# Performance work log

Measured on AMD Instinct MI355X. Metric: run time of the kernel, lower is better.

Reference implementation:

```python
import jax, jax.numpy as jnp
import numpy as np

BN_EPS = 1e-5

def setup_inputs() -> dict:
    key = jax.random.key(0)
    k1, k2 = jax.random.split(key)
    B, C, H, W, K = 256, 2048, 7, 7, 16
    featmap = jax.random.normal(k1, (B, C, H, W), dtype=jnp.float32)
    w16 = jax.random.normal(k2, (K, C), dtype=jnp.float32) * 0.02  # 1x1 conv weight
    bn_gamma = jnp.ones((K,), jnp.float32)
    bn_beta = jnp.zeros((K,), jnp.float32)
    bn_mean = jnp.zeros((K,), jnp.float32)
    bn_var = jnp.ones((K,), jnp.float32)
    return {"featmap": featmap, "w16": w16, "bn_gamma": bn_gamma,
            "bn_beta": bn_beta, "bn_mean": bn_mean, "bn_var": bn_var}

def reference(featmap, w16, bn_gamma, bn_beta, bn_mean, bn_var):
    # featmap: [B, 2048, 7, 7]; 1x1 conv -> featcov16: [B, 16, 7, 7]
    featcov16 = jnp.einsum('bchw,kc->bkhw', featmap, w16)
    # BatchNorm2d(16), inference-style with running stats
    inv = bn_gamma / jnp.sqrt(bn_var + BN_EPS)
    featcov16 = featcov16 * inv[None, :, None, None] + (bn_beta - bn_mean * inv)[None, :, None, None]
    # Loop-free bilinear pooling: original repeats featcov16[:,i] to 2048 ch,
    # multiplies with featmap, and AvgPool2d(7) -> mean over HxW.
    HW = featmap.shape[2] * featmap.shape[3]
    feat_matrix = jnp.einsum('bkhw,bchw->bkc', featcov16, featmap) / HW  # [B,16,2048]
    bp_out_feat = feat_matrix.reshape(feat_matrix.shape[0], -1)  # [B, 32768]
    return bp_out_feat
```

## Files before the change

kernel.cpp:

```cpp
#include <hip/hip_runtime.h>

#define BATCH 256
#define CDIM  2048
#define HW    49
#define KDIM  16


__global__ __launch_bounds__(256) void prep_kernel(
    const float* __restrict__ w16,
    const float* __restrict__ gamma, const float* __restrict__ beta,
    const float* __restrict__ mean,  const float* __restrict__ var,
    float* __restrict__ wT, float* __restrict__ pscr)
{
    const int idx = blockIdx.x * 256 + threadIdx.x;
    if (idx < CDIM * KDIM) {
        const int c = idx >> 4, k = idx & 15;
        const float inv = gamma[k] * rsqrtf(var[k] + 1e-5f) * (1.0f / 49.0f);
        wT[idx] = w16[k * CDIM + c] * inv;
    }
    for (int i = idx; i < BATCH * (HW * KDIM); i += 256 * 256) {
        const int k = i & 15;
        const float inv   = gamma[k] * rsqrtf(var[k] + 1e-5f);
        const float shift = (beta[k] - mean[k] * inv) * (1.0f / 49.0f);
        pscr[i] = shift;
    }
}

__global__ __launch_bounds__(512) void conv_kernel(
    const float* __restrict__ fm, const float* __restrict__ wT,
    float* __restrict__ pscr)
{
    __shared__ float red[8 * KDIM * 52];

    const int tid  = threadIdx.x;
    const int b    = blockIdx.x >> 2;
    const int q    = blockIdx.x & 3;
    const int wav  = __builtin_amdgcn_readfirstlane(tid >> 6);
    const int lane = tid & 63;
    const int hwi  = lane < HW ? lane : HW - 1;
    const int cbase = q * 512 + wav * 64;

    const float*  __restrict__ fmb = fm + (size_t)b * CDIM * HW;
    const float4* __restrict__ wt4 = (const float4*)wT;

    float acc[KDIM];
    #pragma unroll
    for (int k = 0; k < KDIM; ++k) acc[k] = 0.f;

    #pragma unroll 2
    for (int g = 0; g < 64; g += 8) {
        float f[8];
        #pragma unroll
        for (int u = 0; u < 8; ++u)
            f[u] = fmb[(size_t)(cbase + g + u) * HW + hwi];
        #pragma unroll
        for (int u = 0; u < 8; ++u) {
            const int c4 = (cbase + g + u) * 4;
            const float4 w0 = wt4[c4 + 0];
            const float4 w1 = wt4[c4 + 1];
            const float4 w2 = wt4[c4 + 2];
            const float4 w3 = wt4[c4 + 3];
            const float fv = f[u];
            acc[0]  += w0.x * fv; acc[1]  += w0.y * fv; acc[2]  += w0.z * fv; acc[3]  += w0.w * fv;
            acc[4]  += w1.x * fv; acc[5]  += w1.y * fv; acc[6]  += w1.z * fv; acc[7]  += w1.w * fv;
            acc[8]  += w2.x * fv; acc[9]  += w2.y * fv; acc[10] += w2.z * fv; acc[11] += w2.w * fv;
            acc[12] += w3.x * fv; acc[13] += w3.y * fv; acc[14] += w3.z * fv; acc[15] += w3.w * fv;
        }
    }

    if (lane < HW) {
        #pragma unroll
        for (int k = 0; k < KDIM; ++k)
            red[wav * (KDIM * 52) + k * 52 + lane] = acc[k];
    }
    __syncthreads();
    for (int j = tid; j < HW * KDIM; j += 512) {
        const int k = j / HW, hw = j - k * HW;
        float s = 0.f;
        #pragma unroll
        for (int w = 0; w < 8; ++w) s += red[w * (KDIM * 52) + k * 52 + hw];
        atomicAdd(&pscr[(size_t)b * (HW * KDIM) + hw * KDIM + k], s);
    }
}

__global__ __launch_bounds__(256) void bp_kernel(
    const float* __restrict__ fm, const float* __restrict__ pscr,
    float* __restrict__ out)
{
    __shared__ __align__(16) float fs[256 * HW];

    const int tid  = threadIdx.x;
    const int b    = blockIdx.x >> 1;
    const int half = blockIdx.x & 1;

    const float*  __restrict__ fmb = fm + (size_t)b * CDIM * HW;
    const float4* __restrict__ P4  = (const float4*)(pscr + (size_t)b * (HW * KDIM));

    for (int ch = 0; ch < 4; ++ch) {
        const int cb = half * 1024 + ch * 256;
        __syncthreads();
        {
            const float4* src = (const float4*)(fmb + (size_t)cb * HW);
            float4* dst = (float4*)fs;
            for (int i = tid; i < (256 * HW) / 4; i += 256) dst[i] = src[i];
        }
        __syncthreads();

        float acc[KDIM];
        #pragma unroll
        for (int k = 0; k < KDIM; ++k) acc[k] = 0.f;

        const float* row = fs + tid * HW;
        #pragma unroll 7
        for (int hw = 0; hw < HW; ++hw) {
            const float fv = row[hw];
            const float4 p0 = P4[hw * 4 + 0];
            const float4 p1 = P4[hw * 4 + 1];
            const float4 p2 = P4[hw * 4 + 2];
            const float4 p3 = P4[hw * 4 + 3];
            acc[0]  += p0.x * fv; acc[1]  += p0.y * fv; acc[2]  += p0.z * fv; acc[3]  += p0.w * fv;
            acc[4]  += p1.x * fv; acc[5]  += p1.y * fv; acc[6]  += p1.z * fv; acc[7]  += p1.w * fv;
            acc[8]  += p2.x * fv; acc[9]  += p2.y * fv; acc[10] += p2.z * fv; acc[11] += p2.w * fv;
            acc[12] += p3.x * fv; acc[13] += p3.y * fv; acc[14] += p3.z * fv; acc[15] += p3.w * fv;
        }

        float* ob = out + (size_t)b * (KDIM * CDIM) + cb + tid;
        #pragma unroll
        for (int k = 0; k < KDIM; ++k) ob[k * CDIM] = acc[k];
    }
}

extern "C" void kernel_launch(void* const* d_in, const int* in_sizes, int n_in,
                              void* d_out, int out_size, void* d_ws, size_t ws_size,
                              hipStream_t stream) {
    const float* fm    = (const float*)d_in[0];
    const float* w16   = (const float*)d_in[1];
    const float* gamma = (const float*)d_in[2];
    const float* beta  = (const float*)d_in[3];
    const float* mean  = (const float*)d_in[4];
    const float* var   = (const float*)d_in[5];
    float* out  = (float*)d_out;
    float* wT   = (float*)d_ws;
    float* pscr = (float*)d_ws + CDIM * KDIM;

    prep_kernel<<<256, 256, 0, stream>>>(w16, gamma, beta, mean, var, wT, pscr);
    conv_kernel<<<BATCH * 4, 512, 0, stream>>>(fm, wT, pscr);
    bp_kernel<<<BATCH * 2, 256, 0, stream>>>(fm, pscr, out);
}
```

Measured before the change: 224.5 us.

## Replace conv atomics with per-strip partials, LDS direct loads, and finer bp grid

The conv kernel now splits each batch into 8 channel strips and loads each strip straight into LDS with global_load_lds. Each block writes a non-atomic partial result, and a new mid kernel sums the partials and adds the BN shift. This removes the atomicAdd contention and the pscr initialisation in the prep kernel. The bp kernel now uses 8 blocks per batch with one chunk each, which raises parallelism, at the cost of an extra kernel launch and a pass over the partial buffer.

```diff
diff --git a/kernel.cpp b/kernel.cpp
--- a/kernel.cpp
+++ b/kernel.cpp
@@ -5,82 +5,111 @@
 #define HW    49
 #define KDIM  16
 
+#define OSTRIP 8
+#define SC     256
+#define STRIP_B (SC * HW * 4)
+#define NLOAD  (STRIP_B / 1024)
+
+#define GLDS(g, l) __builtin_amdgcn_global_load_lds(                        \
+        (const __attribute__((address_space(1))) unsigned int*)(g),          \
+        (__attribute__((address_space(3))) unsigned int*)(l), 16, 0, 0)
+
 
 __global__ __launch_bounds__(256) void prep_kernel(
     const float* __restrict__ w16,
-    const float* __restrict__ gamma, const float* __restrict__ beta,
-    const float* __restrict__ mean,  const float* __restrict__ var,
-    float* __restrict__ wT, float* __restrict__ pscr)
+    const float* __restrict__ gamma, const float* __restrict__ var,
+    float* __restrict__ wT)
 {
     const int idx = blockIdx.x * 256 + threadIdx.x;
-    if (idx < CDIM * KDIM) {
-        const int c = idx >> 4, k = idx & 15;
-        const float inv = gamma[k] * rsqrtf(var[k] + 1e-5f) * (1.0f / 49.0f);
-        wT[idx] = w16[k * CDIM + c] * inv;
-    }
-    for (int i = idx; i < BATCH * (HW * KDIM); i += 256 * 256) {
-        const int k = i & 15;
-        const float inv   = gamma[k] * rsqrtf(var[k] + 1e-5f);
-        const float shift = (beta[k] - mean[k] * inv) * (1.0f / 49.0f);
-        pscr[i] = shift;
-    }
+    const int c = idx >> 4, k = idx & 15;
+    const float inv = gamma[k] * rsqrtf(var[k] + 1e-5f) * (1.0f / 49.0f);
+    wT[idx] = w16[k * CDIM + c] * inv;
 }
 
-__global__ __launch_bounds__(512) void conv_kernel(
+__global__ __launch_bounds__(256) void conv_kernel(
     const float* __restrict__ fm, const float* __restrict__ wT,
     float* __restrict__ pscr)
 {
-    __shared__ float red[8 * KDIM * 52];
+    __shared__ __align__(16) float fbuf[SC * HW + 4];
+    __shared__ __align__(16) float red[4 * KDIM * 52];
 
     const int tid  = threadIdx.x;
-    const int b    = blockIdx.x >> 2;
-    const int q    = blockIdx.x & 3;
-    const int wav  = __builtin_amdgcn_readfirstlane(tid >> 6);
+    const int b    = blockIdx.x >> 3;
+    const int o    = blockIdx.x & 7;
+    const int wavu = __builtin_amdgcn_readfirstlane(tid >> 6);
     const int lane = tid & 63;
     const int hwi  = lane < HW ? lane : HW - 1;
-    const int cbase = q * 512 + wav * 64;
 
-    const float*  __restrict__ fmb = fm + (size_t)b * CDIM * HW;
-    const float4* __restrict__ wt4 = (const float4*)wT;
+    {
+        const char* gbase = (const char*)fm
+            + (size_t)b * (CDIM * HW * 4) + (size_t)o * STRIP_B;
+        char* lbase = (char*)fbuf;
+        const int nld = (wavu == 0) ? 13 : 12;
+        for (int i = 0; i < nld; ++i) {
+            const int j = wavu + 4 * i;
+            GLDS(gbase + j * 1024 + lane * 16, lbase + j * 1024);
+        }
+    }
+    __syncthreads();
 
     float acc[KDIM];
     #pragma unroll
     for (int k = 0; k < KDIM; ++k) acc[k] = 0.f;
 
-    #pragma unroll 2
-    for (int g = 0; g < 64; g += 8) {
-        float f[8];
-        #pragma unroll
-        for (int u = 0; u < 8; ++u)
-            f[u] = fmb[(size_t)(cbase + g + u) * HW + hwi];
-        #pragma unroll
-        for (int u = 0; u < 8; ++u) {
-            const int c4 = (cbase + g + u) * 4;
-            const float4 w0 = wt4[c4 + 0];
-            const float4 w1 = wt4[c4 + 1];
-            const float4 w2 = wt4[c4 + 2];
-            const float4 w3 = wt4[c4 + 3];
-            const float fv = f[u];
-            acc[0]  += w0.x * fv; acc[1]  += w0.y * fv; acc[2]  += w0.z * fv; acc[3]  += w0.w * fv;
-            acc[4]  += w1.x * fv; acc[5]  += w1.y * fv; acc[6]  += w1.z * fv; acc[7]  += w1.w * fv;
-            acc[8]  += w2.x * fv; acc[9]  += w2.y * fv; acc[10] += w2.z * fv; acc[11] += w2.w * fv;
-            acc[12] += w3.x * fv; acc[13] += w3.y * fv; acc[14] += w3.z * fv; acc[15] += w3.w * fv;
-        }
+    const int cl0 = wavu * 64;
+    const float4* __restrict__ wq = (const float4*)(wT + (size_t)((o * SC + cl0) << 4));
+
+    #pragma unroll 8
+    for (int cc = 0; cc < 64; ++cc) {
+        const float fv = fbuf[(cl0 + cc) * HW + hwi];
+        const float4 w0 = wq[cc * 4 + 0];
+        const float4 w1 = wq[cc * 4 + 1];
+        const float4 w2 = wq[cc * 4 + 2];
+        const float4 w3 = wq[cc * 4 + 3];
+        acc[0]  += w0.x * fv; acc[1]  += w0.y * fv; acc[2]  += w0.z * fv; acc[3]  += w0.w * fv;
+        acc[4]  += w1.x * fv; acc[5]  += w1.y * fv; acc[6]  += w1.z * fv; acc[7]  += w1.w * fv;
+        acc[8]  += w2.x * fv; acc[9]  += w2.y * fv; acc[10] += w2.z * fv; acc[11] += w2.w * fv;
+        acc[12] += w3.x * fv; acc[13] += w3.y * fv; acc[14] += w3.z * fv; acc[15] += w3.w * fv;
     }
 
     if (lane < HW) {
         #pragma unroll
         for (int k = 0; k < KDIM; ++k)
-            red[wav * (KDIM * 52) + k * 52 + lane] = acc[k];
+            red[wavu * (KDIM * 52) + k * 52 + lane] = acc[k];
     }
     __syncthreads();
-    for (int j = tid; j < HW * KDIM; j += 512) {
-        const int k = j / HW, hw = j - k * HW;
-        float s = 0.f;
-        #pragma unroll
-        for (int w = 0; w < 8; ++w) s += red[w * (KDIM * 52) + k * 52 + hw];
-        atomicAdd(&pscr[(size_t)b * (HW * KDIM) + hw * KDIM + k], s);
+    for (int p = tid; p < HW * KDIM; p += 256) {
+        const int k = p / HW, hw = p - k * HW;
+        const int a = k * 52 + hw;
+        const float s = red[a] + red[a + 832] + red[a + 1664] + red[a + 2496];
+        pscr[(size_t)blockIdx.x * 784 + p] = s;
     }
+}
+
+__global__ __launch_bounds__(256) void mid_kernel(
+    float* __restrict__ pscr,
+    const float* __restrict__ gamma, const float* __restrict__ beta,
+    const float* __restrict__ mean,  const float* __restrict__ var)
+{
+    const int tid  = threadIdx.x;
+    const size_t base = (size_t)blockIdx.x * (OSTRIP * 784);
+    float s0 = 0.f, s1 = 0.f, s2 = 0.f, s3 = 0.f;
+
+#define MIDR(SV, R) { const int j = tid + 256 * (R); if (j < 784) {            \
+        const int k = j & 15, hw = j >> 4;                                     \
+        const size_t src = base + k * HW + hw;                                 \
+        float t = 0.f;                                                         \
+        _Pragma("unroll")                                                      \
+        for (int oo = 0; oo < OSTRIP; ++oo) t += pscr[src + oo * 784];         \
+        const float inv = gamma[k] * rsqrtf(var[k] + 1e-5f);                   \
+        SV = t + (beta[k] - mean[k] * inv) * (1.0f / 49.0f); } }
+    MIDR(s0, 0) MIDR(s1, 1) MIDR(s2, 2) MIDR(s3, 3)
+#undef MIDR
+    __syncthreads();
+    if (tid < 784)        pscr[base + tid]       = s0;
+    if (tid + 256 < 784)  pscr[base + tid + 256] = s1;
+    if (tid + 512 < 784)  pscr[base + tid + 512] = s2;
+    if (tid + 768 < 784)  pscr[base + tid + 768] = s3;
 }
 
 __global__ __launch_bounds__(256) void bp_kernel(
@@ -89,45 +118,40 @@
 {
     __shared__ __align__(16) float fs[256 * HW];
 
-    const int tid  = threadIdx.x;
-    const int b    = blockIdx.x >> 1;
-    const int half = blockIdx.x & 1;
+    const int tid = threadIdx.x;
+    const int b   = blockIdx.x >> 3;
+    const int oc  = (blockIdx.x & 7) * 256;
 
-    const float*  __restrict__ fmb = fm + (size_t)b * CDIM * HW;
-    const float4* __restrict__ P4  = (const float4*)(pscr + (size_t)b * (HW * KDIM));
+    {
+        const float4* src = (const float4*)(fm + ((size_t)b * CDIM + oc) * HW);
+        float4* dst = (float4*)fs;
+        for (int i = tid; i < (256 * HW) / 4; i += 256) dst[i] = src[i];
+    }
+    __syncthreads();
 
-    for (int ch = 0; ch < 4; ++ch) {
-        const int cb = half * 1024 + ch * 256;
-        __syncthreads();
-        {
-            const float4* src = (const float4*)(fmb + (size_t)cb * HW);
-            float4* dst = (float4*)fs;
-            for (int i = tid; i < (256 * HW) / 4; i += 256) dst[i] = src[i];
-        }
-        __syncthreads();
+    const float4* __restrict__ P4 = (const float4*)(pscr + (size_t)b * (OSTRIP * 784));
 
-        float acc[KDIM];
-        #pragma unroll
-        for (int k = 0; k < KDIM; ++k) acc[k] = 0.f;
+    float acc[KDIM];
+    #pragma unroll
+    for (int k = 0; k < KDIM; ++k) acc[k] = 0.f;
 
-        const float* row = fs + tid * HW;
-        #pragma unroll 7
-        for (int hw = 0; hw < HW; ++hw) {
-            const float fv = row[hw];
-            const float4 p0 = P4[hw * 4 + 0];
-            const float4 p1 = P4[hw * 4 + 1];
-            const float4 p2 = P4[hw * 4 + 2];
-            const float4 p3 = P4[hw * 4 + 3];
-            acc[0]  += p0.x * fv; acc[1]  += p0.y * fv; acc[2]  += p0.z * fv; acc[3]  += p0.w * fv;
-            acc[4]  += p1.x * fv; acc[5]  += p1.y * fv; acc[6]  += p1.z * fv; acc[7]  += p1.w * fv;
-            acc[8]  += p2.x * fv; acc[9]  += p2.y * fv; acc[10] += p2.z * fv; acc[11] += p2.w * fv;
-            acc[12] += p3.x * fv; acc[13] += p3.y * fv; acc[14] += p3.z * fv; acc[15] += p3.w * fv;
-        }
+    const float* row = fs + tid * HW;
+    #pragma unroll
+    for (int hw = 0; hw < HW; ++hw) {
+        const float fv = row[hw];
+        const float4 p0 = P4[hw * 4 + 0];
+        const float4 p1 = P4[hw * 4 + 1];
+        const float4 p2 = P4[hw * 4 + 2];
+        const float4 p3 = P4[hw * 4 + 3];
+        acc[0]  += p0.x * fv; acc[1]  += p0.y * fv; acc[2]  += p0.z * fv; acc[3]  += p0.w * fv;
+        acc[4]  += p1.x * fv; acc[5]  += p1.y * fv; acc[6]  += p1.z * fv; acc[7]  += p1.w * fv;
+        acc[8]  += p2.x * fv; acc[9]  += p2.y * fv; acc[10] += p2.z * fv; acc[11] += p2.w * fv;
+        acc[12] += p3.x * fv; acc[13] += p3.y * fv; acc[14] += p3.z * fv; acc[15] += p3.w * fv;
+    }
 
-        float* ob = out + (size_t)b * (KDIM * CDIM) + cb + tid;
-        #pragma unroll
-        for (int k = 0; k < KDIM; ++k) ob[k * CDIM] = acc[k];
-    }
+    float* ob = out + (size_t)b * (KDIM * CDIM) + oc + tid;
+    #pragma unroll
+    for (int k = 0; k < KDIM; ++k) ob[k * CDIM] = acc[k];
 }
 
 extern "C" void kernel_launch(void* const* d_in, const int* in_sizes, int n_in,
@@ -143,7 +167,8 @@
     float* wT   = (float*)d_ws;
     float* pscr = (float*)d_ws + CDIM * KDIM;
 
-    prep_kernel<<<256, 256, 0, stream>>>(w16, gamma, beta, mean, var, wT, pscr);
-    conv_kernel<<<BATCH * 4, 512, 0, stream>>>(fm, wT, pscr);
-    bp_kernel<<<BATCH * 2, 256, 0, stream>>>(fm, pscr, out);
+    prep_kernel<<<128, 256, 0, stream>>>(w16, gamma, var, wT);
+    conv_kernel<<<BATCH * OSTRIP, 256, 0, stream>>>(fm, wT, pscr);
+    mid_kernel<<<BATCH, 256, 0, stream>>>(pscr, gamma, beta, mean, var);
+    bp_kernel<<<BATCH * 8, 256, 0, stream>>>(fm, pscr, out);
 }
```

New measurement: 220.5 us. About the same (-1.8%).
